# Performance work log

Hardware: AMD Instinct MI355X
Metric: run time of the kernel (lower is better)

The kernel has to match this reference:

```python
import jax, jax.numpy as jnp
import numpy as np
from functools import partial

N_NODES = 100000
N_EDGES = 3200000
F_IN, H1, H2, C_OUT = 128, 64, 32, 2


def setup_inputs() -> dict:
    key = jax.random.key(0)
    ks = jax.random.split(key, 8)
    x = jax.random.normal(ks[0], (N_NODES, F_IN), dtype=jnp.float32)
    edge_index = jax.random.randint(ks[1], (2, N_EDGES), 0, N_NODES, dtype=jnp.int64)
    def glorot(k, fan_in, fan_out):
        s = jnp.sqrt(6.0 / (fan_in + fan_out))
        return jax.random.uniform(k, (fan_in, fan_out), jnp.float32, -s, s)
    return {
        "x": x,
        "edge_index": edge_index,
        "W1": glorot(ks[2], F_IN, H1), "b1": jnp.zeros((H1,), jnp.float32),
        "W2": glorot(ks[3], H1, H2),   "b2": jnp.zeros((H2,), jnp.float32),
        "W3": glorot(ks[4], H2, C_OUT), "b3": jnp.zeros((C_OUT,), jnp.float32),
    }


def _gcn_norm(edge_index, num_nodes):
    # add self-loops, compute symmetric normalization D^{-1/2} (A+I) D^{-1/2}
    loop = jnp.arange(num_nodes, dtype=edge_index.dtype)
    src = jnp.concatenate([edge_index[0], loop])
    dst = jnp.concatenate([edge_index[1], loop])
    deg = jax.ops.segment_sum(jnp.ones_like(dst, dtype=jnp.float32), dst,
                              num_segments=num_nodes)
    dinv = jax.lax.rsqrt(deg)  # deg >= 1 because of self-loops
    norm = dinv[src] * dinv[dst]  # [E + N]
    return src, dst, norm


def _gcn_conv(x, W, b, src, dst, norm, num_nodes):
    # PyG GCNConv: linear transform, then normalized scatter-aggregate, then bias
    xw = x @ W                                   # [N, F_out]
    msg = xw[src] * norm[:, None]                # [E+N, F_out] gather + scale
    out = jax.ops.segment_sum(msg, dst, num_segments=num_nodes)
    return out + b


def reference(x, edge_index, W1, b1, W2, b2, W3, b3):
    n = x.shape[0]
    src, dst, norm = _gcn_norm(edge_index, n)
    h = jax.nn.relu(_gcn_conv(x, W1, b1, src, dst, norm, n))
    # dropout is identity in eval mode
    h = jax.nn.relu(_gcn_conv(h, W2, b2, src, dst, norm, n))
    h = _gcn_conv(h, W3, b3, src, dst, norm, n)
    return jax.nn.log_softmax(h, axis=1)
```

## Files before the change

kernel.cpp:

```cpp
#include <hip/hip_runtime.h>
#include <hip/hip_bf16.h>
#include <math.h>

constexpr int N = 100000;
constexpr int E = 3200000;
constexpr int FIN = 128, H1 = 64, H2 = 32, COUT = 2;

constexpr int BUK_SHIFT = 6;
constexpr int BUK_NODES = 64;
constexpr int NBUK = (N + BUK_NODES - 1) / BUK_NODES;
constexpr int CAP = 2560;
constexpr int SEG_SHIFT = 14;
constexpr int NSEG = 7;
constexpr int KEYS = BUK_NODES * NSEG;
constexpr int RP_STR = BUK_NODES + 1;

constexpr int MS_TPB = 1024;
constexpr int MS_EPT = 24;
constexpr int CHUNK = MS_TPB * MS_EPT;
constexpr int MS_WGS = (E + CHUNK - 1) / CHUNK;

__global__ void k_initcur(int* __restrict__ gcursor) {
    int i = blockIdx.x * blockDim.x + threadIdx.x;
    if (i < NBUK) gcursor[i] = i * CAP;
}

__global__ __launch_bounds__(MS_TPB)
void k_mslice(const int* __restrict__ src, const int* __restrict__ dst,
              int* __restrict__ gcursor, unsigned* __restrict__ ebuf) {
    __shared__ int cnt[NBUK];
    __shared__ int base[NBUK];
    const int t = threadIdx.x;
    for (int i = t; i < NBUK; i += MS_TPB) cnt[i] = 0;
    __syncthreads();
    const int e0 = blockIdx.x * CHUNK;

    int rb[MS_EPT];
    unsigned rv[MS_EPT];
#pragma unroll
    for (int j = 0; j < MS_EPT; ++j) {
        int e = e0 + j * MS_TPB + t;
        if (e < E) {
            int d = dst[e];
            int b = d >> BUK_SHIFT;
            rb[j] = b;
            rv[j] = (unsigned)src[e] | ((unsigned)(d & (BUK_NODES - 1)) << 17);
            atomicAdd(&cnt[b], 1);
        } else {
            rb[j] = -1; rv[j] = 0;
        }
    }
    __syncthreads();
    for (int i = t; i < NBUK; i += MS_TPB) {
        int c = cnt[i];
        base[i] = c ? atomicAdd(&gcursor[i], c) : 0;
    }
    __syncthreads();
    for (int i = t; i < NBUK; i += MS_TPB) cnt[i] = 0;
    __syncthreads();
#pragma unroll
    for (int j = 0; j < MS_EPT; ++j) {
        int b = rb[j];
        if (b >= 0) {
            int r = atomicAdd(&cnt[b], 1);
            int p = base[b] + r;
            if (p < (b + 1) * CAP) ebuf[p] = rv[j];
        }
    }
}

__global__ __launch_bounds__(256)
void k_build(const int* __restrict__ gcursor, unsigned* __restrict__ ebuf,
             int* __restrict__ rp, float* __restrict__ dinv) {
    __shared__ unsigned ent[CAP];
    __shared__ int cnt[512];
    __shared__ int sa[512];
    __shared__ int sb[512];
    __shared__ int cur[512];
    const int b = blockIdx.x;
    const int t = threadIdx.x;
    int fill = gcursor[b] - b * CAP;
    if (fill > CAP) fill = CAP;
    const int gbase = b * CAP;

    cnt[t] = 0; cnt[t + 256] = 0;
    __syncthreads();
    for (int j = t; j < fill; j += 256) {
        unsigned v = ebuf[gbase + j];
        ent[j] = v;
        int key = (int)(v >> 17) * NSEG + (int)((v & 0x1FFFFu) >> SEG_SHIFT);
        atomicAdd(&cnt[key], 1);
    }
    __syncthreads();
    sa[t] = cnt[t]; sa[t + 256] = cnt[t + 256];
    __syncthreads();
    int* pin = sa; int* pout = sb;
    for (int off = 1; off < 512; off <<= 1) {
        pout[t]       = pin[t]       + ((t >= off)       ? pin[t - off]       : 0);
        pout[t + 256] = pin[t + 256] + ((t + 256 >= off) ? pin[t + 256 - off] : 0);
        __syncthreads();
        int* tmp = pin; pin = pout; pout = tmp;
    }
    {
        int ex0 = pin[t] - cnt[t];
        int ex1 = pin[t + 256] - cnt[t + 256];
        cur[t] = gbase + ex0;
        cur[t + 256] = gbase + ex1;
        if (t < KEYS && (t % NSEG) == 0)
            rp[b * RP_STR + t / NSEG] = gbase + ex0;
        int k2 = t + 256;
        if (k2 < KEYS && (k2 % NSEG) == 0)
            rp[b * RP_STR + k2 / NSEG] = gbase + ex1;
        if (t == 0) rp[b * RP_STR + BUK_NODES] = gbase + fill;
    }
    if (t < BUK_NODES) {
        int deg = 0;
#pragma unroll
        for (int s = 0; s < NSEG; ++s) deg += cnt[t * NSEG + s];
        int node = (b << BUK_SHIFT) + t;
        if (node < N) dinv[node] = rsqrtf((float)deg + 1.0f);
    }
    __syncthreads();
    for (int j = t; j < fill; j += 256) {
        unsigned v = ent[j];
        int key = (int)(v >> 17) * NSEG + (int)((v & 0x1FFFFu) >> SEG_SHIFT);
        int p = atomicAdd(&cur[key], 1);
        ebuf[p] = v & 0x1FFFFu;
    }
}

template<int FI, int FO>
__global__ __launch_bounds__(256)
void k_gemm_tile_bf(const float* __restrict__ h, const float* __restrict__ Wg,
                    const float* __restrict__ dinv, __hip_bfloat16* __restrict__ y) {
    constexpr int TX  = FO / 4;
    constexpr int TY  = 256 / TX;
    constexpr int RPT = 64 / TY;
    constexpr int XS  = 68;
    constexpr int KQ  = FI / 4;

    __shared__ float xsT[FI][XS];

    const int tid = threadIdx.x;
    const int tx = tid % TX;
    const int ty = tid / TX;
    const int row0 = blockIdx.x * 64;

    for (int idx = tid; idx < 64 * KQ; idx += 256) {
        int g   = idx / 8;
        int rlo = idx % 8;
        int k4  = g % KQ;
        int rhi = g / KQ;
        int r   = rlo + 8 * rhi;
        int row = row0 + r;
        float4 v = make_float4(0.f, 0.f, 0.f, 0.f);
        if (row < N) v = *(const float4*)(h + (size_t)row * FI + 4 * k4);
        xsT[4 * k4 + 0][r] = v.x;
        xsT[4 * k4 + 1][r] = v.y;
        xsT[4 * k4 + 2][r] = v.z;
        xsT[4 * k4 + 3][r] = v.w;
    }
    __syncthreads();

    float acc[RPT][4];
#pragma unroll
    for (int i = 0; i < RPT; ++i)
#pragma unroll
        for (int c = 0; c < 4; ++c) acc[i][c] = 0.0f;

#pragma unroll 4
    for (int k = 0; k < FI; ++k) {
        const float4 wv = *(const float4*)(Wg + (size_t)k * FO + 4 * tx);
        float xv[RPT];
        if constexpr (RPT == 4) {
            float4 t = *(const float4*)&xsT[k][4 * ty];
            xv[0] = t.x; xv[1] = t.y; xv[2] = t.z; xv[3] = t.w;
        } else {
            float2 t = *(const float2*)&xsT[k][2 * ty];
            xv[0] = t.x; xv[1] = t.y;
        }
#pragma unroll
        for (int i = 0; i < RPT; ++i) {
            acc[i][0] = fmaf(xv[i], wv.x, acc[i][0]);
            acc[i][1] = fmaf(xv[i], wv.y, acc[i][1]);
            acc[i][2] = fmaf(xv[i], wv.z, acc[i][2]);
            acc[i][3] = fmaf(xv[i], wv.w, acc[i][3]);
        }
    }

#pragma unroll
    for (int i = 0; i < RPT; ++i) {
        int row = row0 + ty * RPT + i;
        if (row >= N) continue;
        float di = dinv[row];
        auto cvt = [](float f) -> unsigned short {
            __hip_bfloat16 b = __float2bfloat16(f);
            return *reinterpret_cast<unsigned short*>(&b);
        };
        ushort4 pk;
        pk.x = cvt(di * acc[i][0]);
        pk.y = cvt(di * acc[i][1]);
        pk.z = cvt(di * acc[i][2]);
        pk.w = cvt(di * acc[i][3]);
        *(ushort4*)&y[(size_t)row * FO + 4 * tx] = pk;
    }
}

template<int FI, int FO, int ROWS>
__global__ __launch_bounds__(FO * ROWS)
void k_gemm_scale(const float* __restrict__ h, const float* __restrict__ W,
                  const float* __restrict__ dinv, float* __restrict__ y) {
    __shared__ float xs[ROWS][FI];
    const int j = threadIdx.x;
    const int r = threadIdx.y;
    const int row0 = blockIdx.x * ROWS;
    const int tid = r * FO + j;
    constexpr int NT = FO * ROWS;
    for (int t = tid; t < ROWS * FI; t += NT) {
        int rr = t / FI, kk = t % FI;
        int row = row0 + rr;
        xs[rr][kk] = (row < N) ? h[(size_t)row * FI + kk] : 0.0f;
    }
    __syncthreads();
    const int row = row0 + r;
    if (row >= N) return;
    float acc = 0.0f;
#pragma unroll
    for (int k = 0; k < FI; ++k)
        acc = fmaf(xs[r][k], W[k * FO + j], acc);
    y[(size_t)row * FO + j] = dinv[row] * acc;
}

template<int F, bool RELU>
__global__ __launch_bounds__(256)
void k_aggregate_bf(const int* __restrict__ rp, const unsigned* __restrict__ csr,
                    const __hip_bfloat16* __restrict__ y, const float* __restrict__ dinv,
                    const float* __restrict__ b, float* __restrict__ out) {
    constexpr int LPN = F / 2;
    constexpr int NPB = 256 / LPN;
    const int fp = threadIdx.x;
    const int n = blockIdx.x * NPB + threadIdx.y;
    if (n >= N) return;
    const unsigned* yw = (const unsigned*)y;

    auto load2 = [&](int s) -> float2 {
        unsigned u = yw[(size_t)s * LPN + fp];
        float2 v;
        v.x = __uint_as_float(u << 16);
        v.y = __uint_as_float(u & 0xffff0000u);
        return v;
    };

    const int rb = (n >> BUK_SHIFT) * RP_STR + (n & (BUK_NODES - 1));
    const int j0 = rp[rb], j1 = rp[rb + 1];
    float2 acc = load2(n);
    int j = j0;
    for (; j + 8 <= j1; j += 8) {
        int s0 = (int)csr[j],     s1 = (int)csr[j + 1], s2 = (int)csr[j + 2], s3 = (int)csr[j + 3];
        int s4 = (int)csr[j + 4], s5 = (int)csr[j + 5], s6 = (int)csr[j + 6], s7 = (int)csr[j + 7];
        float2 v0 = load2(s0), v1 = load2(s1), v2 = load2(s2), v3 = load2(s3);
        float2 v4 = load2(s4), v5 = load2(s5), v6 = load2(s6), v7 = load2(s7);
        acc.x += ((v0.x + v1.x) + (v2.x + v3.x)) + ((v4.x + v5.x) + (v6.x + v7.x));
        acc.y += ((v0.y + v1.y) + (v2.y + v3.y)) + ((v4.y + v5.y) + (v6.y + v7.y));
    }
    for (; j < j1; ++j) {
        float2 v = load2((int)csr[j]);
        acc.x += v.x; acc.y += v.y;
    }
    const float di = dinv[n];
    float o0 = fmaf(di, acc.x, b[2 * fp]);
    float o1 = fmaf(di, acc.y, b[2 * fp + 1]);
    if (RELU) { o0 = fmaxf(o0, 0.0f); o1 = fmaxf(o1, 0.0f); }
    float2 res; res.x = o0; res.y = o1;
    *(float2*)&out[(size_t)n * F + 2 * fp] = res;
}

__global__ __launch_bounds__(256)
void k_final(const int* __restrict__ rp, const unsigned* __restrict__ csr,
             const float* __restrict__ y, const float* __restrict__ dinv,
             const float* __restrict__ bias, float* __restrict__ out) {
    const int c = threadIdx.x;
    const int n = blockIdx.x * 128 + threadIdx.y;
    float z = 0.0f;
    if (n < N) {
        const int rb = (n >> BUK_SHIFT) * RP_STR + (n & (BUK_NODES - 1));
        int j = rp[rb];
        const int j1 = rp[rb + 1];
        float acc = y[2 * n + c];
        for (; j + 4 <= j1; j += 4) {
            int s0 = (int)csr[j], s1 = (int)csr[j + 1], s2 = (int)csr[j + 2], s3 = (int)csr[j + 3];
            float a0 = y[2 * s0 + c], a1 = y[2 * s1 + c];
            float a2 = y[2 * s2 + c], a3 = y[2 * s3 + c];
            acc += (a0 + a1) + (a2 + a3);
        }
        for (; j < j1; ++j) acc += y[2 * (int)csr[j] + c];
        z = fmaf(dinv[n], acc, bias[c]);
    }
    float zo = __shfl_xor(z, 1);
    if (n < N) {
        float m = fmaxf(z, zo);
        float lse = m + logf(expf(z - m) + expf(zo - m));
        out[2 * n + c] = z - lse;
    }
}

extern "C" void kernel_launch(void* const* d_in, const int* in_sizes, int n_in,
                              void* d_out, int out_size, void* d_ws, size_t ws_size,
                              hipStream_t stream) {
    const float* x   = (const float*)d_in[0];
    const int*   ei  = (const int*)d_in[1];
    const float* W1  = (const float*)d_in[2];
    const float* b1  = (const float*)d_in[3];
    const float* W2  = (const float*)d_in[4];
    const float* b2  = (const float*)d_in[5];
    const float* W3  = (const float*)d_in[6];
    const float* b3  = (const float*)d_in[7];
    float* out = (float*)d_out;

    const int* src = ei;
    const int* dst = ei + E;

    char* p = (char*)d_ws;
    float*    dinv    = (float*)p;    p += (size_t)N * 4;
    int*      gcursor = (int*)p;      p += (size_t)NBUK * 4;
    int*      rp      = (int*)p;      p += (size_t)NBUK * RP_STR * 4;
    unsigned* ebuf    = (unsigned*)p; p += (size_t)NBUK * CAP * 4;
    char*     bufA    = p;            p += (size_t)N * 64 * 4;
    char*     bufB    = p;            p += (size_t)N * 64 * 4;

    __hip_bfloat16* y1 = (__hip_bfloat16*)bufA;
    float*          h1 = (float*)bufB;
    __hip_bfloat16* y2 = (__hip_bfloat16*)bufA;
    float*          h2 = (float*)(bufA + (size_t)N * H2 * 2);
    float*          y3 = (float*)bufB;

    k_initcur<<<(NBUK + 255) / 256, 256, 0, stream>>>(gcursor);
    k_mslice <<<MS_WGS, MS_TPB, 0, stream>>>(src, dst, gcursor, ebuf);
    k_build  <<<NBUK, 256, 0, stream>>>(gcursor, ebuf, rp, dinv);

    k_gemm_tile_bf<FIN, H1><<<(N + 63) / 64, 256, 0, stream>>>(x, W1, dinv, y1);
    k_aggregate_bf<H1, true><<<(N + 7) / 8, dim3(32, 8), 0, stream>>>(rp, ebuf, y1, dinv, b1, h1);

    k_gemm_tile_bf<H1, H2><<<(N + 63) / 64, 256, 0, stream>>>(h1, W2, dinv, y2);
    k_aggregate_bf<H2, true><<<(N + 15) / 16, dim3(16, 16), 0, stream>>>(rp, ebuf, y2, dinv, b2, h2);

    k_gemm_scale<H2, COUT, 128><<<(N + 127) / 128, dim3(COUT, 128), 0, stream>>>(h2, W3, dinv, y3);
    k_final<<<(N + 127) / 128, dim3(2, 128), 0, stream>>>(rp, ebuf, y3, dinv, b3, out);
}
```

Measured before the change: 379.6 us.

## Reorder bucket CSR segment-major and aggregate per source segment with syncs

The build step now sorts edges in each destination bucket by source-segment first and then by node, and it stores a row pointer for every (segment, node) key. The aggregation kernels hold accumulators for 80 nodes in shared memory. They walk the seven source-index segments in lockstep with a barrier after each, so all gathers at any moment hit a limited window of the feature table. The aim is better L2/cache locality for the random gathers. The cost is more row-pointer reads, a shared-memory accumulator, and block-wide syncs that can stall on load imbalance.

```diff
diff --git a/kernel.cpp b/kernel.cpp
--- a/kernel.cpp
+++ b/kernel.cpp
@@ -12,8 +12,8 @@
 constexpr int CAP = 2560;
 constexpr int SEG_SHIFT = 14;
 constexpr int NSEG = 7;
-constexpr int KEYS = BUK_NODES * NSEG;
-constexpr int RP_STR = BUK_NODES + 1;
+constexpr int KEYS = NSEG * BUK_NODES;
+constexpr int RP2_STR = KEYS + 1;
 
 constexpr int MS_TPB = 1024;
 constexpr int MS_EPT = 24;
@@ -71,7 +71,7 @@
 
 __global__ __launch_bounds__(256)
 void k_build(const int* __restrict__ gcursor, unsigned* __restrict__ ebuf,
-             int* __restrict__ rp, float* __restrict__ dinv) {
+             int* __restrict__ rp2, float* __restrict__ dinv) {
     __shared__ unsigned ent[CAP];
     __shared__ int cnt[512];
     __shared__ int sa[512];
@@ -88,7 +88,7 @@
     for (int j = t; j < fill; j += 256) {
         unsigned v = ebuf[gbase + j];
         ent[j] = v;
-        int key = (int)(v >> 17) * NSEG + (int)((v & 0x1FFFFu) >> SEG_SHIFT);
+        int key = (int)((v & 0x1FFFFu) >> SEG_SHIFT) * BUK_NODES + (int)(v >> 17);
         atomicAdd(&cnt[key], 1);
     }
     __syncthreads();
@@ -106,24 +106,22 @@
         int ex1 = pin[t + 256] - cnt[t + 256];
         cur[t] = gbase + ex0;
         cur[t + 256] = gbase + ex1;
-        if (t < KEYS && (t % NSEG) == 0)
-            rp[b * RP_STR + t / NSEG] = gbase + ex0;
+        if (t < KEYS) rp2[b * RP2_STR + t] = gbase + ex0;
         int k2 = t + 256;
-        if (k2 < KEYS && (k2 % NSEG) == 0)
-            rp[b * RP_STR + k2 / NSEG] = gbase + ex1;
-        if (t == 0) rp[b * RP_STR + BUK_NODES] = gbase + fill;
+        if (k2 < KEYS) rp2[b * RP2_STR + k2] = gbase + ex1;
+        if (t == 0) rp2[b * RP2_STR + KEYS] = gbase + fill;
     }
     if (t < BUK_NODES) {
         int deg = 0;
 #pragma unroll
-        for (int s = 0; s < NSEG; ++s) deg += cnt[t * NSEG + s];
+        for (int s = 0; s < NSEG; ++s) deg += cnt[s * BUK_NODES + t];
         int node = (b << BUK_SHIFT) + t;
         if (node < N) dinv[node] = rsqrtf((float)deg + 1.0f);
     }
     __syncthreads();
     for (int j = t; j < fill; j += 256) {
         unsigned v = ent[j];
-        int key = (int)(v >> 17) * NSEG + (int)((v & 0x1FFFFu) >> SEG_SHIFT);
+        int key = (int)((v & 0x1FFFFu) >> SEG_SHIFT) * BUK_NODES + (int)(v >> 17);
         int p = atomicAdd(&cur[key], 1);
         ebuf[p] = v & 0x1FFFFu;
     }
@@ -231,16 +229,19 @@
     y[(size_t)row * FO + j] = dinv[row] * acc;
 }
 
-template<int F, bool RELU>
+template<int F, bool RELU, int NPB>
 __global__ __launch_bounds__(256)
-void k_aggregate_bf(const int* __restrict__ rp, const unsigned* __restrict__ csr,
-                    const __hip_bfloat16* __restrict__ y, const float* __restrict__ dinv,
-                    const float* __restrict__ b, float* __restrict__ out) {
+void k_agg_seg(const int* __restrict__ rp2, const unsigned* __restrict__ csr,
+               const __hip_bfloat16* __restrict__ y, const float* __restrict__ dinv,
+               const float* __restrict__ bias, float* __restrict__ out) {
     constexpr int LPN = F / 2;
-    constexpr int NPB = 256 / LPN;
-    const int fp = threadIdx.x;
-    const int n = blockIdx.x * NPB + threadIdx.y;
-    if (n >= N) return;
+    constexpr int NPG = 256 / LPN;
+    constexpr int NG  = NPB / NPG;
+    __shared__ float acc[NPB][F];
+    const int tid = threadIdx.x;
+    const int fp  = tid & (LPN - 1);
+    const int ny  = tid / LPN;
+    const int n0  = blockIdx.x * NPB;
     const unsigned* yw = (const unsigned*)y;
 
     auto load2 = [&](int s) -> float2 {
@@ -251,49 +252,82 @@
         return v;
     };
 
-    const int rb = (n >> BUK_SHIFT) * RP_STR + (n & (BUK_NODES - 1));
-    const int j0 = rp[rb], j1 = rp[rb + 1];
-    float2 acc = load2(n);
-    int j = j0;
-    for (; j + 8 <= j1; j += 8) {
-        int s0 = (int)csr[j],     s1 = (int)csr[j + 1], s2 = (int)csr[j + 2], s3 = (int)csr[j + 3];
-        int s4 = (int)csr[j + 4], s5 = (int)csr[j + 5], s6 = (int)csr[j + 6], s7 = (int)csr[j + 7];
-        float2 v0 = load2(s0), v1 = load2(s1), v2 = load2(s2), v3 = load2(s3);
-        float2 v4 = load2(s4), v5 = load2(s5), v6 = load2(s6), v7 = load2(s7);
-        acc.x += ((v0.x + v1.x) + (v2.x + v3.x)) + ((v4.x + v5.x) + (v6.x + v7.x));
-        acc.y += ((v0.y + v1.y) + (v2.y + v3.y)) + ((v4.y + v5.y) + (v6.y + v7.y));
-    }
-    for (; j < j1; ++j) {
-        float2 v = load2((int)csr[j]);
-        acc.x += v.x; acc.y += v.y;
-    }
-    const float di = dinv[n];
-    float o0 = fmaf(di, acc.x, b[2 * fp]);
-    float o1 = fmaf(di, acc.y, b[2 * fp + 1]);
-    if (RELU) { o0 = fmaxf(o0, 0.0f); o1 = fmaxf(o1, 0.0f); }
-    float2 res; res.x = o0; res.y = o1;
-    *(float2*)&out[(size_t)n * F + 2 * fp] = res;
+    for (int i = tid; i < NPB * LPN; i += 256) {
+        int nl = i / LPN, f2 = i - nl * LPN;
+        int n = n0 + nl;
+        float2 v = make_float2(0.f, 0.f);
+        if (n < N) {
+            unsigned u = yw[(size_t)n * LPN + f2];
+            v.x = __uint_as_float(u << 16);
+            v.y = __uint_as_float(u & 0xffff0000u);
+        }
+        acc[nl][2 * f2]     = v.x;
+        acc[nl][2 * f2 + 1] = v.y;
+    }
+    __syncthreads();
+
+    for (int s = 0; s < NSEG; ++s) {
+        for (int g = 0; g < NG; ++g) {
+            const int nl = g * NPG + ny;
+            const int n  = n0 + nl;
+            if (n < N) {
+                const int kb = (n >> BUK_SHIFT) * RP2_STR + s * BUK_NODES + (n & (BUK_NODES - 1));
+                int j        = rp2[kb];
+                const int j1 = rp2[kb + 1];
+                float ax = 0.f, ay = 0.f;
+                for (; j + 4 <= j1; j += 4) {
+                    int s0 = (int)csr[j],     s1 = (int)csr[j + 1];
+                    int s2 = (int)csr[j + 2], s3 = (int)csr[j + 3];
+                    float2 v0 = load2(s0), v1 = load2(s1), v2 = load2(s2), v3 = load2(s3);
+                    ax += (v0.x + v1.x) + (v2.x + v3.x);
+                    ay += (v0.y + v1.y) + (v2.y + v3.y);
+                }
+                for (; j < j1; ++j) {
+                    float2 v = load2((int)csr[j]);
+                    ax += v.x; ay += v.y;
+                }
+                acc[nl][2 * fp]     += ax;
+                acc[nl][2 * fp + 1] += ay;
+            }
+        }
+        __syncthreads();
+    }
+
+    for (int i = tid; i < NPB * LPN; i += 256) {
+        int nl = i / LPN, f2 = i - nl * LPN;
+        int n = n0 + nl;
+        if (n < N) {
+            float di = dinv[n];
+            float o0 = fmaf(di, acc[nl][2 * f2],     bias[2 * f2]);
+            float o1 = fmaf(di, acc[nl][2 * f2 + 1], bias[2 * f2 + 1]);
+            if (RELU) { o0 = fmaxf(o0, 0.0f); o1 = fmaxf(o1, 0.0f); }
+            *(float2*)&out[(size_t)n * F + 2 * f2] = make_float2(o0, o1);
+        }
+    }
 }
 
 __global__ __launch_bounds__(256)
-void k_final(const int* __restrict__ rp, const unsigned* __restrict__ csr,
+void k_final(const int* __restrict__ rp2, const unsigned* __restrict__ csr,
              const float* __restrict__ y, const float* __restrict__ dinv,
              const float* __restrict__ bias, float* __restrict__ out) {
     const int c = threadIdx.x;
     const int n = blockIdx.x * 128 + threadIdx.y;
     float z = 0.0f;
     if (n < N) {
-        const int rb = (n >> BUK_SHIFT) * RP_STR + (n & (BUK_NODES - 1));
-        int j = rp[rb];
-        const int j1 = rp[rb + 1];
+        const int base = (n >> BUK_SHIFT) * RP2_STR + (n & (BUK_NODES - 1));
         float acc = y[2 * n + c];
-        for (; j + 4 <= j1; j += 4) {
-            int s0 = (int)csr[j], s1 = (int)csr[j + 1], s2 = (int)csr[j + 2], s3 = (int)csr[j + 3];
-            float a0 = y[2 * s0 + c], a1 = y[2 * s1 + c];
-            float a2 = y[2 * s2 + c], a3 = y[2 * s3 + c];
-            acc += (a0 + a1) + (a2 + a3);
-        }
-        for (; j < j1; ++j) acc += y[2 * (int)csr[j] + c];
+#pragma unroll
+        for (int s = 0; s < NSEG; ++s) {
+            int j        = rp2[base + s * BUK_NODES];
+            const int j1 = rp2[base + s * BUK_NODES + 1];
+            for (; j + 4 <= j1; j += 4) {
+                int s0 = (int)csr[j], s1 = (int)csr[j + 1], s2 = (int)csr[j + 2], s3 = (int)csr[j + 3];
+                float a0 = y[2 * s0 + c], a1 = y[2 * s1 + c];
+                float a2 = y[2 * s2 + c], a3 = y[2 * s3 + c];
+                acc += (a0 + a1) + (a2 + a3);
+            }
+            for (; j < j1; ++j) acc += y[2 * (int)csr[j] + c];
+        }
         z = fmaf(dinv[n], acc, bias[c]);
     }
     float zo = __shfl_xor(z, 1);
@@ -323,7 +357,7 @@
     char* p = (char*)d_ws;
     float*    dinv    = (float*)p;    p += (size_t)N * 4;
     int*      gcursor = (int*)p;      p += (size_t)NBUK * 4;
-    int*      rp      = (int*)p;      p += (size_t)NBUK * RP_STR * 4;
+    int*      rp2     = (int*)p;      p += (size_t)NBUK * RP2_STR * 4;
     unsigned* ebuf    = (unsigned*)p; p += (size_t)NBUK * CAP * 4;
     char*     bufA    = p;            p += (size_t)N * 64 * 4;
     char*     bufB    = p;            p += (size_t)N * 64 * 4;
@@ -336,14 +370,14 @@
 
     k_initcur<<<(NBUK + 255) / 256, 256, 0, stream>>>(gcursor);
     k_mslice <<<MS_WGS, MS_TPB, 0, stream>>>(src, dst, gcursor, ebuf);
-    k_build  <<<NBUK, 256, 0, stream>>>(gcursor, ebuf, rp, dinv);
+    k_build  <<<NBUK, 256, 0, stream>>>(gcursor, ebuf, rp2, dinv);
 
     k_gemm_tile_bf<FIN, H1><<<(N + 63) / 64, 256, 0, stream>>>(x, W1, dinv, y1);
-    k_aggregate_bf<H1, true><<<(N + 7) / 8, dim3(32, 8), 0, stream>>>(rp, ebuf, y1, dinv, b1, h1);
+    k_agg_seg<H1, true, 80><<<(N + 79) / 80, 256, 0, stream>>>(rp2, ebuf, y1, dinv, b1, h1);
 
     k_gemm_tile_bf<H1, H2><<<(N + 63) / 64, 256, 0, stream>>>(h1, W2, dinv, y2);
-    k_aggregate_bf<H2, true><<<(N + 15) / 16, dim3(16, 16), 0, stream>>>(rp, ebuf, y2, dinv, b2, h2);
+    k_agg_seg<H2, true, 80><<<(N + 79) / 80, 256, 0, stream>>>(rp2, ebuf, y2, dinv, b2, h2);
 
     k_gemm_scale<H2, COUT, 128><<<(N + 127) / 128, dim3(COUT, 128), 0, stream>>>(h2, W3, dinv, y3);
-    k_final<<<(N + 127) / 128, dim3(2, 128), 0, stream>>>(rp, ebuf, y3, dinv, b3, out);
-}
+    k_final<<<(N + 127) / 128, dim3(2, 128), 0, stream>>>(rp2, ebuf, y3, dinv, b3, out);
+}
```

After: 490.3 us. 29.1% more time.
